# Kernel optimization log

Hardware: AMD Instinct MI355X
Metric: run time of the kernel (lower is better)

The kernel has to match this reference:

```python
import jax, jax.numpy as jnp
import numpy as np

A_MIN = 0.001
EPS = 1e-08


def setup_inputs() -> dict:
    key = jax.random.key(0)
    k1, k2, k3, k4 = jax.random.split(key, 4)
    B, O, I = 512, 1024, 512
    x = jax.random.normal(k1, (B, I), dtype=jnp.float32)
    translation = jax.random.uniform(k2, (O, I), dtype=jnp.float32, minval=-1.0, maxval=1.0)
    scale_raw = jax.random.uniform(k3, (O, I), dtype=jnp.float32, minval=-2.0, maxval=0.0)
    weights = jax.random.normal(k4, (O, I), dtype=jnp.float32) * (1.0 / np.sqrt(I))
    return {"x": x, "translation": translation, "scale_raw": scale_raw, "weights": weights}


def reference(x, translation, scale_raw, weights):
    # x: (B, I); params: (O, I)
    scale = A_MIN + jax.nn.softplus(scale_raw)  # (O, I)
    # s: (B, O, I) broadcast intermediate
    s = (x[:, None, :] - translation[None, :, :]) / (scale[None, :, :] + EPS)
    s2 = s * s
    wavelet = (1.0 - s2) * jnp.exp(-0.5 * s2)  # mexican hat
    y = jnp.einsum('oi,boi->bo', weights, wavelet)  # reduce over in_features
    return y
```

## Files before the change

kernel.cpp:

```cpp
#include <hip/hip_runtime.h>
#include <hip/hip_bf16.h>


#define WL_A_MIN 0.001f
#define WL_EPS   1e-8f

constexpr int WL_B = 512;
constexpr int WL_O = 1024;
constexpr int WL_I = 512;

#define WL_SQK  0.84932180553704583800f
#define WL_IK   1.38629436111989061883f
#define WL_L2E  1.44269504088896340736f
#define WL_LN2  0.69314718055994530942f

typedef float v2f __attribute__((ext_vector_type(2)));

struct P3 { float nti, inv, w; };

__device__ __forceinline__ float fast_exp2(float a) {
#if __has_builtin(__builtin_amdgcn_exp2f)
    return __builtin_amdgcn_exp2f(a);
#else
    return exp2f(a);
#endif
}
__device__ __forceinline__ float fast_log2(float a) {
#if __has_builtin(__builtin_amdgcn_logf)
    return __builtin_amdgcn_logf(a);
#else
    return __log2f(a);
#endif
}
__device__ __forceinline__ float fast_rcp(float a) {
#if __has_builtin(__builtin_amdgcn_rcpf)
    return __builtin_amdgcn_rcpf(a);
#else
    return 1.0f / a;
#endif
}

__global__ __launch_bounds__(256) void wl_prep(
    const float* __restrict__ translation,
    const float* __restrict__ scale_raw,
    const float* __restrict__ weights,
    P3* __restrict__ pT3)
{
    const int lane   = threadIdx.x & 63;
    const int ic     = threadIdx.x >> 6;
    const int o      = blockIdx.x * 64 + lane;
    const int i_base = blockIdx.y * 64 + ic * 16;

    #pragma unroll 4
    for (int k = 0; k < 16; ++k) {
        int i  = i_base + k;
        int gi = o * WL_I + i;
        float t  = translation[gi];
        float sr = scale_raw[gi];
        float w  = weights[gi];
        float ex    = fast_exp2(sr * WL_L2E);
        float sp    = fast_log2(1.0f + ex) * WL_LN2;
        float inv   = fast_rcp(WL_A_MIN + sp + WL_EPS);
        float inv_s = inv * WL_SQK;
        P3 pv; pv.nti = -t * inv_s; pv.inv = inv_s; pv.w = w;
        pT3[(size_t)i * WL_O + o] = pv;
    }
}

__global__ __launch_bounds__(512, 4) void wl_main(
    const float* __restrict__ x,
    const P3* __restrict__ pT3,
    float* __restrict__ out)
{
    __shared__ float smem[WL_I * 16];

    const int tid  = threadIdx.x;
    const int lane = tid & 63;
    const int wid  = tid >> 6;
    const int o    = blockIdx.x * 64 + lane;
    const int b0   = blockIdx.y * 16;

    {
        const int b_l = tid & 15;
        const int seg = tid >> 4;
        const float* xg = &x[(b0 + b_l) * WL_I + seg * 16];
        #pragma unroll
        for (int q = 0; q < 4; ++q) {
            float4 v = *reinterpret_cast<const float4*>(xg + q * 4);
            int i0 = seg * 16 + q * 4;
            smem[(i0 + 0) * 16 + b_l] = v.x;
            smem[(i0 + 1) * 16 + b_l] = v.y;
            smem[(i0 + 2) * 16 + b_l] = v.z;
            smem[(i0 + 3) * 16 + b_l] = v.w;
        }
    }
    __syncthreads();

    const int oct = wid & 1;
    const int iq  = wid >> 1;
    const P3*    pp   = pT3 + o;
    const float* xrow = &smem[oct * 8];

    v2f aE0 = {0.f,0.f}, aE1 = {0.f,0.f}, aE2 = {0.f,0.f}, aE3 = {0.f,0.f};
    v2f aU0 = {0.f,0.f}, aU1 = {0.f,0.f}, aU2 = {0.f,0.f}, aU3 = {0.f,0.f};

    const int iBeg = iq * 128;
    #pragma unroll 4
    for (int ii = 0; ii < 128; ++ii) {
        const int i = iBeg + ii;
        P3 p = pp[(size_t)i * WL_O];
        float4 xa = *reinterpret_cast<const float4*>(xrow + i * 16);
        float4 xb = *reinterpret_cast<const float4*>(xrow + i * 16 + 4);

        v2f nti = {p.nti, p.nti};
        v2f inv = {p.inv, p.inv};
        v2f wv  = {p.w,  p.w};

        v2f x01 = {xa.x, xa.y};
        v2f x23 = {xa.z, xa.w};
        v2f x45 = {xb.x, xb.y};
        v2f x67 = {xb.z, xb.w};

        v2f s0 = __builtin_elementwise_fma(x01, inv, nti);
        v2f s1 = __builtin_elementwise_fma(x23, inv, nti);
        v2f s2 = __builtin_elementwise_fma(x45, inv, nti);
        v2f s3 = __builtin_elementwise_fma(x67, inv, nti);
        v2f u0 = s0 * s0;
        v2f u1 = s1 * s1;
        v2f u2 = s2 * s2;
        v2f u3 = s3 * s3;
        v2f e0 = {fast_exp2(-u0.x), fast_exp2(-u0.y)};
        v2f e1 = {fast_exp2(-u1.x), fast_exp2(-u1.y)};
        v2f e2 = {fast_exp2(-u2.x), fast_exp2(-u2.y)};
        v2f e3 = {fast_exp2(-u3.x), fast_exp2(-u3.y)};
        aE0 = __builtin_elementwise_fma(wv, e0, aE0);
        aE1 = __builtin_elementwise_fma(wv, e1, aE1);
        aE2 = __builtin_elementwise_fma(wv, e2, aE2);
        aE3 = __builtin_elementwise_fma(wv, e3, aE3);
        v2f ue0 = u0 * e0;
        v2f ue1 = u1 * e1;
        v2f ue2 = u2 * e2;
        v2f ue3 = u3 * e3;
        aU0 = __builtin_elementwise_fma(wv, ue0, aU0);
        aU1 = __builtin_elementwise_fma(wv, ue1, aU1);
        aU2 = __builtin_elementwise_fma(wv, ue2, aU2);
        aU3 = __builtin_elementwise_fma(wv, ue3, aU3);
    }

    __syncthreads();
    constexpr int RS = 20;
    if (iq != 0) {
        float4* dst = reinterpret_cast<float4*>(
            &smem[(((iq - 1) * 2 + oct) * 64 + lane) * RS]);
        dst[0] = make_float4(aE0.x, aE0.y, aE1.x, aE1.y);
        dst[1] = make_float4(aE2.x, aE2.y, aE3.x, aE3.y);
        dst[2] = make_float4(aU0.x, aU0.y, aU1.x, aU1.y);
        dst[3] = make_float4(aU2.x, aU2.y, aU3.x, aU3.y);
    }
    __syncthreads();
    if (iq == 0) {
        float E[8] = {aE0.x, aE0.y, aE1.x, aE1.y, aE2.x, aE2.y, aE3.x, aE3.y};
        float U[8] = {aU0.x, aU0.y, aU1.x, aU1.y, aU2.x, aU2.y, aU3.x, aU3.y};
        #pragma unroll
        for (int q = 1; q < 4; ++q) {
            const float4* src = reinterpret_cast<const float4*>(
                &smem[(((q - 1) * 2 + oct) * 64 + lane) * RS]);
            float4 v0 = src[0], v1 = src[1], v2 = src[2], v3 = src[3];
            E[0] += v0.x; E[1] += v0.y; E[2] += v0.z; E[3] += v0.w;
            E[4] += v1.x; E[5] += v1.y; E[6] += v1.z; E[7] += v1.w;
            U[0] += v2.x; U[1] += v2.y; U[2] += v2.z; U[3] += v2.w;
            U[4] += v3.x; U[5] += v3.y; U[6] += v3.z; U[7] += v3.w;
        }
        const int b = b0 + oct * 8;
        #pragma unroll
        for (int k = 0; k < 8; ++k)
            out[(size_t)(b + k) * WL_O + o] = fmaf(-WL_IK, U[k], E[k]);
    }
}

extern "C" void kernel_launch(void* const* d_in, const int* in_sizes, int n_in,
                              void* d_out, int out_size, void* d_ws, size_t ws_size,
                              hipStream_t stream) {
    const float* x           = (const float*)d_in[0];
    const float* translation = (const float*)d_in[1];
    const float* scale_raw   = (const float*)d_in[2];
    const float* weights     = (const float*)d_in[3];
    float*       out         = (float*)d_out;
    P3*          pT3         = (P3*)d_ws;

    wl_prep<<<dim3(WL_O / 64, WL_I / 64), dim3(256), 0, stream>>>(
        translation, scale_raw, weights, pT3);

    wl_main<<<dim3(WL_O / 64, WL_B / 16), dim3(512), 0, stream>>>(
        x, pT3, out);
}
```

Measured before the change: 111.1 us.

## Coalesce prep transpose via LDS and shrink main tile to 8 batches

The prep kernel now loads each parameter with coalesced float4 reads, computes the softplus-derived terms, and transposes through shared memory so the pT3 stores are also coalesced. The main kernel drops from 16 to 8 batch rows per block, and each of its 8 waves now covers 64 input features instead of splitting work by batch-octet and feature-quarter. The cross-wave reduction becomes a two-level tree through shared memory. Less shared memory per block and launch bounds raised to 8 are meant to increase occupancy, but each parameter load is now reused across only 8 batch rows instead of 16, doubling pT3 traffic.

```diff
diff --git a/kernel.cpp b/kernel.cpp
--- a/kernel.cpp
+++ b/kernel.cpp
@@ -1,5 +1,4 @@
 #include <hip/hip_runtime.h>
-#include <hip/hip_bf16.h>
 
 
 #define WL_A_MIN 0.001f
@@ -46,71 +45,85 @@
     const float* __restrict__ weights,
     P3* __restrict__ pT3)
 {
-    const int lane   = threadIdx.x & 63;
-    const int ic     = threadIdx.x >> 6;
-    const int o      = blockIdx.x * 64 + lane;
-    const int i_base = blockIdx.y * 64 + ic * 16;
-
-    #pragma unroll 4
-    for (int k = 0; k < 16; ++k) {
-        int i  = i_base + k;
-        int gi = o * WL_I + i;
-        float t  = translation[gi];
-        float sr = scale_raw[gi];
-        float w  = weights[gi];
-        float ex    = fast_exp2(sr * WL_L2E);
-        float sp    = fast_log2(1.0f + ex) * WL_LN2;
-        float inv   = fast_rcp(WL_A_MIN + sp + WL_EPS);
-        float inv_s = inv * WL_SQK;
-        P3 pv; pv.nti = -t * inv_s; pv.inv = inv_s; pv.w = w;
-        pT3[(size_t)i * WL_O + o] = pv;
-    }
-}
-
-__global__ __launch_bounds__(512, 4) void wl_main(
+    __shared__ P3 lds[16 * 64];
+    const int t  = threadIdx.x;
+    const int o0 = blockIdx.x * 64;
+    const int i0 = blockIdx.y * 16;
+
+    {
+        const int o_l = t >> 2;
+        const int iq  = t & 3;
+        const size_t g = (size_t)(o0 + o_l) * WL_I + (i0 + iq * 4);
+        const float4 tv = *reinterpret_cast<const float4*>(translation + g);
+        const float4 sv = *reinterpret_cast<const float4*>(scale_raw   + g);
+        const float4 wv = *reinterpret_cast<const float4*>(weights     + g);
+        const float tt[4] = {tv.x, tv.y, tv.z, tv.w};
+        const float ss[4] = {sv.x, sv.y, sv.z, sv.w};
+        const float ww[4] = {wv.x, wv.y, wv.z, wv.w};
+        #pragma unroll
+        for (int j = 0; j < 4; ++j) {
+            float ex  = fast_exp2(ss[j] * WL_L2E);
+            float sp  = fast_log2(1.0f + ex) * WL_LN2;
+            float inv = fast_rcp(WL_A_MIN + sp + WL_EPS) * WL_SQK;
+            P3 pv; pv.nti = -tt[j] * inv; pv.inv = inv; pv.w = ww[j];
+            lds[(iq * 4 + j) * 64 + o_l] = pv;
+        }
+    }
+    __syncthreads();
+    {
+        const int o_l = t & 63;
+        const int r   = t >> 6;
+        #pragma unroll
+        for (int j = 0; j < 4; ++j) {
+            const int i_l = r * 4 + j;
+            pT3[(size_t)(i0 + i_l) * WL_O + (o0 + o_l)] = lds[i_l * 64 + o_l];
+        }
+    }
+}
+
+__global__ __launch_bounds__(512, 8) void wl_main(
     const float* __restrict__ x,
     const P3* __restrict__ pT3,
     float* __restrict__ out)
 {
-    __shared__ float smem[WL_I * 16];
+    __shared__ float smem[5120];
 
     const int tid  = threadIdx.x;
     const int lane = tid & 63;
     const int wid  = tid >> 6;
     const int o    = blockIdx.x * 64 + lane;
-    const int b0   = blockIdx.y * 16;
+    const int b0   = blockIdx.y * 8;
 
     {
-        const int b_l = tid & 15;
-        const int seg = tid >> 4;
-        const float* xg = &x[(b0 + b_l) * WL_I + seg * 16];
-        #pragma unroll
-        for (int q = 0; q < 4; ++q) {
-            float4 v = *reinterpret_cast<const float4*>(xg + q * 4);
-            int i0 = seg * 16 + q * 4;
-            smem[(i0 + 0) * 16 + b_l] = v.x;
-            smem[(i0 + 1) * 16 + b_l] = v.y;
-            smem[(i0 + 2) * 16 + b_l] = v.z;
-            smem[(i0 + 3) * 16 + b_l] = v.w;
-        }
-    }
-    __syncthreads();
-
-    const int oct = wid & 1;
-    const int iq  = wid >> 1;
-    const P3*    pp   = pT3 + o;
-    const float* xrow = &smem[oct * 8];
+        const int b_l = tid & 7;
+        const int seg = tid >> 3;
+        const float* xg = &x[(size_t)(b0 + b_l) * WL_I + seg * 8];
+        const float4 v0 = *reinterpret_cast<const float4*>(xg);
+        const float4 v1 = *reinterpret_cast<const float4*>(xg + 4);
+        const int base = seg * 64 + b_l;
+        smem[base +  0] = v0.x;
+        smem[base +  8] = v0.y;
+        smem[base + 16] = v0.z;
+        smem[base + 24] = v0.w;
+        smem[base + 32] = v1.x;
+        smem[base + 40] = v1.y;
+        smem[base + 48] = v1.z;
+        smem[base + 56] = v1.w;
+    }
+    __syncthreads();
+
+    const P3*    pp = pT3 + (size_t)(wid * 64) * WL_O + o;
+    const float* xr = &smem[wid * 64 * 8];
 
     v2f aE0 = {0.f,0.f}, aE1 = {0.f,0.f}, aE2 = {0.f,0.f}, aE3 = {0.f,0.f};
     v2f aU0 = {0.f,0.f}, aU1 = {0.f,0.f}, aU2 = {0.f,0.f}, aU3 = {0.f,0.f};
 
-    const int iBeg = iq * 128;
     #pragma unroll 4
-    for (int ii = 0; ii < 128; ++ii) {
-        const int i = iBeg + ii;
-        P3 p = pp[(size_t)i * WL_O];
-        float4 xa = *reinterpret_cast<const float4*>(xrow + i * 16);
-        float4 xb = *reinterpret_cast<const float4*>(xrow + i * 16 + 4);
+    for (int ii = 0; ii < 64; ++ii) {
+        const P3 p = *pp;  pp += WL_O;
+        const float4 xa = *reinterpret_cast<const float4*>(xr);
+        const float4 xb = *reinterpret_cast<const float4*>(xr + 4);
+        xr += 8;
 
         v2f nti = {p.nti, p.nti};
         v2f inv = {p.inv, p.inv};
@@ -149,32 +162,46 @@
 
     __syncthreads();
     constexpr int RS = 20;
-    if (iq != 0) {
-        float4* dst = reinterpret_cast<float4*>(
-            &smem[(((iq - 1) * 2 + oct) * 64 + lane) * RS]);
+    if (wid >= 4) {
+        float4* dst = reinterpret_cast<float4*>(&smem[((wid - 4) * 64 + lane) * RS]);
         dst[0] = make_float4(aE0.x, aE0.y, aE1.x, aE1.y);
         dst[1] = make_float4(aE2.x, aE2.y, aE3.x, aE3.y);
         dst[2] = make_float4(aU0.x, aU0.y, aU1.x, aU1.y);
         dst[3] = make_float4(aU2.x, aU2.y, aU3.x, aU3.y);
     }
     __syncthreads();
-    if (iq == 0) {
+    if (wid < 4) {
+        const float4* src = reinterpret_cast<const float4*>(&smem[(wid * 64 + lane) * RS]);
+        const float4 v0 = src[0], v1 = src[1], v2 = src[2], v3 = src[3];
+        aE0.x += v0.x; aE0.y += v0.y; aE1.x += v0.z; aE1.y += v0.w;
+        aE2.x += v1.x; aE2.y += v1.y; aE3.x += v1.z; aE3.y += v1.w;
+        aU0.x += v2.x; aU0.y += v2.y; aU1.x += v2.z; aU1.y += v2.w;
+        aU2.x += v3.x; aU2.y += v3.y; aU3.x += v3.z; aU3.y += v3.w;
+    }
+    __syncthreads();
+    if (wid >= 1 && wid < 4) {
+        float4* dst = reinterpret_cast<float4*>(&smem[((wid - 1) * 64 + lane) * RS]);
+        dst[0] = make_float4(aE0.x, aE0.y, aE1.x, aE1.y);
+        dst[1] = make_float4(aE2.x, aE2.y, aE3.x, aE3.y);
+        dst[2] = make_float4(aU0.x, aU0.y, aU1.x, aU1.y);
+        dst[3] = make_float4(aU2.x, aU2.y, aU3.x, aU3.y);
+    }
+    __syncthreads();
+    if (wid == 0) {
         float E[8] = {aE0.x, aE0.y, aE1.x, aE1.y, aE2.x, aE2.y, aE3.x, aE3.y};
         float U[8] = {aU0.x, aU0.y, aU1.x, aU1.y, aU2.x, aU2.y, aU3.x, aU3.y};
         #pragma unroll
-        for (int q = 1; q < 4; ++q) {
-            const float4* src = reinterpret_cast<const float4*>(
-                &smem[(((q - 1) * 2 + oct) * 64 + lane) * RS]);
-            float4 v0 = src[0], v1 = src[1], v2 = src[2], v3 = src[3];
+        for (int q = 0; q < 3; ++q) {
+            const float4* src = reinterpret_cast<const float4*>(&smem[(q * 64 + lane) * RS]);
+            const float4 v0 = src[0], v1 = src[1], v2 = src[2], v3 = src[3];
             E[0] += v0.x; E[1] += v0.y; E[2] += v0.z; E[3] += v0.w;
             E[4] += v1.x; E[5] += v1.y; E[6] += v1.z; E[7] += v1.w;
             U[0] += v2.x; U[1] += v2.y; U[2] += v2.z; U[3] += v2.w;
             U[4] += v3.x; U[5] += v3.y; U[6] += v3.z; U[7] += v3.w;
         }
-        const int b = b0 + oct * 8;
         #pragma unroll
         for (int k = 0; k < 8; ++k)
-            out[(size_t)(b + k) * WL_O + o] = fmaf(-WL_IK, U[k], E[k]);
+            out[(size_t)(b0 + k) * WL_O + o] = fmaf(-WL_IK, U[k], E[k]);
     }
 }
 
@@ -188,9 +215,9 @@
     float*       out         = (float*)d_out;
     P3*          pT3         = (P3*)d_ws;
 
-    wl_prep<<<dim3(WL_O / 64, WL_I / 64), dim3(256), 0, stream>>>(
+    wl_prep<<<dim3(WL_O / 64, WL_I / 16), dim3(256), 0, stream>>>(
         translation, scale_raw, weights, pT3);
 
-    wl_main<<<dim3(WL_O / 64, WL_B / 16), dim3(512), 0, stream>>>(
+    wl_main<<<dim3(WL_O / 64, WL_B / 8), dim3(512), 0, stream>>>(
         x, pT3, out);
 }
```

Result: no change. 109.7 us (-1.2%).
